# Kernel optimization log

Measured on AMD Instinct MI355X. Metric: run time of the kernel, lower is better.

Reference implementation:

```python
import jax, jax.numpy as jnp
import numpy as np

B, C, T = 8, 512, 1024
H = 8
D = C // H          # head_dim = 64
K = 64              # max_rel_dist
REL = 2 * K + 1     # 129


def setup_inputs() -> dict:
    key = jax.random.key(0)
    ks = jax.random.split(key, 12)
    s = 0.02
    return {
        "x": jax.random.normal(ks[0], (B, C, T), jnp.float32),
        "x_mask": jnp.ones((B, 1, T), jnp.float32),
        "W_q": jax.random.normal(ks[1], (C, C), jnp.float32) * s,
        "b_q": jnp.zeros((C,), jnp.float32),
        "W_k": jax.random.normal(ks[2], (C, C), jnp.float32) * s,
        "b_k": jnp.zeros((C,), jnp.float32),
        "W_v": jax.random.normal(ks[3], (C, C), jnp.float32) * s,
        "b_v": jnp.zeros((C,), jnp.float32),
        "W_o": jax.random.normal(ks[4], (C, C), jnp.float32) * s,
        "b_o": jnp.zeros((C,), jnp.float32),
        "emb_rel_k": jax.random.normal(ks[5], (REL, D), jnp.float32) * 0.01,
        "emb_rel_v": jax.random.normal(ks[6], (REL, D), jnp.float32) * 0.01,
    }


def _conv1x1(x, W, b):
    # Conv1d with kernel_size=1: (B,C,T) x (Cout,Cin) -> (B,Cout,T)
    return jnp.einsum("oc,bct->bot", W, x) + b[None, :, None]


def _shape_heads(x):
    # (B,C,T) -> (B,H,T,D)
    b = x.shape[0]
    return x.reshape(b, H, D, T).transpose(0, 1, 3, 2)


def reference(x, x_mask, W_q, b_q, W_k, b_k, W_v, b_v, W_o, b_o, emb_rel_k, emb_rel_v):
    q = _shape_heads(_conv1x1(x, W_q, b_q))  # (B,H,T,D)
    k = _shape_heads(_conv1x1(x, W_k, b_k))
    v = _shape_heads(_conv1x1(x, W_v, b_v))

    # relative position indices: clamp(j - i, -K, K) + K  -> (T,T)
    pos = jnp.arange(T)
    rel_idx = jnp.clip(pos[None, :] - pos[:, None], -K, K) + K

    # scores: scaled QK^T plus unscaled relative-key term (faithful to source)
    attn = jnp.einsum("bhid,bhjd->bhij", q, k) / (D ** 0.5)
    rel_k_tt = emb_rel_k[rel_idx]            # (T,T,D)
    attn = attn + jnp.einsum("bhid,ijd->bhij", q, rel_k_tt)

    # key mask: positions with x_mask <= 0 get -1e9
    key_mask = (x_mask <= 0).reshape(x.shape[0], 1, 1, T)
    attn = jnp.where(key_mask, -1e9, attn)
    attn = jax.nn.softmax(attn, axis=-1)     # dropout p=0.0 -> identity

    y = jnp.einsum("bhij,bhjd->bhid", attn, v)
    rel_v_tt = emb_rel_v[rel_idx]            # (T,T,D)
    y = y + jnp.einsum("bhij,ijd->bhid", attn, rel_v_tt)

    # (B,H,T,D) -> (B,H,D,T) -> (B,C,T)
    y = y.transpose(0, 1, 3, 2).reshape(x.shape[0], C, T)
    y = _conv1x1(y, W_o, b_o)
    return y * x_mask
```

## Files before the change

kernel.cpp:

```cpp
#include <hip/hip_runtime.h>

#define B_   8
#define C_   512
#define T_   1024
#define H_   8
#define D_   64
#define K_   64
#define REL_ 129

typedef unsigned short u16;
typedef __attribute__((ext_vector_type(8))) short short8;
typedef __attribute__((ext_vector_type(4))) float f32x4;

__device__ __forceinline__ float b2f(u16 u) {
    return __uint_as_float(((unsigned)u) << 16);
}
__device__ __forceinline__ u16 f2b(float f) {
    unsigned x = __float_as_uint(f);
    x += 0x7fffu + ((x >> 16) & 1u);
    return (u16)(x >> 16);
}

__global__ __launch_bounds__(256) void cast_all_kernel(
    const float* __restrict__ x,
    const float* __restrict__ Wq, const float* __restrict__ Wk,
    const float* __restrict__ Wv, const float* __restrict__ Wo,
    const float* __restrict__ erk, const float* __restrict__ erv,
    u16* __restrict__ xt, u16* __restrict__ Wh,
    u16* __restrict__ ervt, u16* __restrict__ erkb)
{
    __shared__ u16 tile[64][72];
    const int blk = blockIdx.x;
    const int tid = threadIdx.x;
    if (blk < 1024) {
        const int t0 = (blk & 15) * 64, c0 = ((blk >> 4) & 7) * 64, b = blk >> 7;
        const int f = tid & 15, r0 = tid >> 4;
#pragma unroll
        for (int p = 0; p < 4; ++p) {
            const int c = r0 + p * 16;
            const float4 v = *(const float4*)(x + ((size_t)b * C_ + c0 + c) * T_ + t0 + f * 4);
            tile[c][f * 4 + 0] = f2b(v.x);
            tile[c][f * 4 + 1] = f2b(v.y);
            tile[c][f * 4 + 2] = f2b(v.z);
            tile[c][f * 4 + 3] = f2b(v.w);
        }
        __syncthreads();
#pragma unroll
        for (int p = 0; p < 4; ++p) {
            const int t = r0 + p * 16;
            ushort4 u;
            u.x = tile[f * 4 + 0][t];
            u.y = tile[f * 4 + 1][t];
            u.z = tile[f * 4 + 2][t];
            u.w = tile[f * 4 + 3][t];
            *(ushort4*)(xt + ((size_t)b * T_ + t0 + t) * C_ + c0 + f * 4) = u;
        }
    } else if (blk < 2048) {
        const int gid = (blk - 1024) * 256 + tid;
        const int s = gid >> 16;
        const int off = (gid & 65535) * 4;
        const float* W = (s == 0) ? Wq : (s == 1) ? Wk : (s == 2) ? Wv : Wo;
        const float4 v = *(const float4*)(W + off);
        ushort4 u;
        u.x = f2b(v.x); u.y = f2b(v.y); u.z = f2b(v.z); u.w = f2b(v.w);
        *(ushort4*)(Wh + ((size_t)s << 18) + off) = u;
    } else {
        const int idx = (blk - 2048) * 256 + tid;
        if (idx < 64 * 160) {
            const int d = idx / 160, rel = idx % 160;
            ervt[idx] = (rel < REL_) ? f2b(erv[rel * D_ + d]) : (u16)0;
        } else {
            const int j = idx - 64 * 160;
            if (j < REL_ * D_) erkb[j] = f2b(erk[j]);
        }
    }
}

__global__ __launch_bounds__(256) void proj_mfma(
    const u16* __restrict__ xt, const u16* __restrict__ Wh,
    const float* __restrict__ bq, const float* __restrict__ bk, const float* __restrict__ bv,
    u16* __restrict__ qh, u16* __restrict__ kh, u16* __restrict__ vt)
{
    __shared__ u16 Wt[64][72];

    const int t0 = blockIdx.x * 128;
    const int h  = blockIdx.y;
    const int sel = blockIdx.z >> 3;
    const int b   = blockIdx.z & 7;
    const int tid = threadIdx.x, wave = tid >> 6, lane = tid & 63;
    const int quad = lane >> 4, l16 = lane & 15;

    const u16* Wbase = Wh + ((size_t)sel << 18) + ((size_t)(h * 64) << 9);
    const u16* A0 = xt + (((size_t)b * T_ + t0 + wave * 16 + l16) << 9);
    const u16* A1 = A0 + ((size_t)64 << 9);

    const int so = tid >> 2;
    const int sc = (tid & 3) * 16;
    const u16* wsrc = Wbase + ((size_t)so << 9) + sc;

    f32x4 acc[2][4];
#pragma unroll
    for (int gg = 0; gg < 2; ++gg)
#pragma unroll
        for (int nt = 0; nt < 4; ++nt) acc[gg][nt] = (f32x4){0.f, 0.f, 0.f, 0.f};

    uint4 wv0 = *(const uint4*)(wsrc);
    uint4 wv1 = *(const uint4*)(wsrc + 8);
#pragma unroll 1
    for (int i = 0; i < 8; ++i) {
        const int c0 = i * 64;
        __syncthreads();
        *(uint4*)&Wt[so][sc] = wv0;
        *(uint4*)&Wt[so][sc + 8] = wv1;
        __syncthreads();
        if (i < 7) {
            wv0 = *(const uint4*)(wsrc + c0 + 64);
            wv1 = *(const uint4*)(wsrc + c0 + 72);
        }
#pragma unroll
        for (int kk = 0; kk < 64; kk += 32) {
            const short8 af0 = *(const short8*)(A0 + c0 + kk + quad * 8);
            const short8 af1 = *(const short8*)(A1 + c0 + kk + quad * 8);
#pragma unroll
            for (int nt = 0; nt < 4; ++nt) {
                const short8 bf = *(const short8*)(&Wt[nt * 16 + l16][kk + quad * 8]);
                acc[0][nt] = __builtin_amdgcn_mfma_f32_16x16x32_bf16(af0, bf, acc[0][nt], 0, 0, 0);
                acc[1][nt] = __builtin_amdgcn_mfma_f32_16x16x32_bf16(af1, bf, acc[1][nt], 0, 0, 0);
            }
        }
    }

    const int bh = b * 8 + h;
    if (sel == 2) {
#pragma unroll
        for (int gg = 0; gg < 2; ++gg) {
            __syncthreads();
#pragma unroll
            for (int nt = 0; nt < 4; ++nt) {
                const int d = nt * 16 + l16;
                const float bo = bv[h * 64 + d];
#pragma unroll
                for (int rix = 0; rix < 4; ++rix) {
                    const int tl = wave * 16 + quad * 4 + rix;
                    Wt[d][tl] = f2b(acc[gg][nt][rix] + bo);
                }
            }
            __syncthreads();
            const int row = tid >> 2;
            const int seg = (tid & 3) * 16;
            const uint4 v0 = *(const uint4*)&Wt[row][seg];
            const uint4 v1 = *(const uint4*)&Wt[row][seg + 8];
            u16* vdst = vt + (((size_t)bh * 64 + row) << 10) + t0 + gg * 64 + seg;
            *(uint4*)(vdst) = v0;
            *(uint4*)(vdst + 8) = v1;
        }
    } else {
        const float* bias = sel ? bk : bq;
        u16* dst = sel ? kh : qh;
#pragma unroll
        for (int nt = 0; nt < 4; ++nt) {
            const int d = nt * 16 + l16;
            const float bo = bias[h * 64 + d];
#pragma unroll
            for (int gg = 0; gg < 2; ++gg)
#pragma unroll
                for (int rix = 0; rix < 4; ++rix) {
                    const int t = t0 + gg * 64 + wave * 16 + quad * 4 + rix;
                    dst[(((size_t)bh * T_ + t) << 6) + d] = f2b(acc[gg][nt][rix] + bo);
                }
        }
    }
}

__global__ __launch_bounds__(256, 2) void attn_kernel(
    const u16* __restrict__ qh, const u16* __restrict__ kh, const u16* __restrict__ vt,
    const u16* __restrict__ erkb, const u16* __restrict__ ervt,
    const float* __restrict__ xmask, u16* __restrict__ yf)
{
    __shared__ u16   Sb[32][1032];
    __shared__ u16   sw[32][168];
    __shared__ float red[4][32][2];
    __shared__ float invrow[32];

    const int gid = blockIdx.x;
    const int x8 = gid & 7, r5 = gid >> 3;
    const int bh = x8 + 8 * (r5 >> 5);
    const int i0 = (r5 & 31) * 32;
    const int b = bh >> 3, h = bh & 7;
    const int tid = threadIdx.x, wave = tid >> 6, lane = tid & 63;
    const int quad = lane >> 4, l16 = lane & 15;

    const float LOG2E = 1.4426950408889634f;
    const float SC    = 0.125f * 1.4426950408889634f;

    short8 qa[2][2];
#pragma unroll
    for (int g = 0; g < 2; ++g) {
        const u16* qrow = qh + (((size_t)bh * T_ + i0 + g * 16 + l16) << 6);
        qa[g][0] = *(const short8*)(qrow + quad * 8);
        qa[g][1] = *(const short8*)(qrow + 32 + quad * 8);
    }

    for (int tile = wave; tile < 9; tile += 4) {
        const int rel = tile * 16 + l16;
        const int rl = rel > 128 ? 128 : rel;
        const u16* ep = erkb + rl * 64 + quad * 8;
        const short8 b0 = *(const short8*)(ep);
        const short8 b1 = *(const short8*)(ep + 32);
#pragma unroll
        for (int g = 0; g < 2; ++g) {
            f32x4 m = {0.f, 0.f, 0.f, 0.f};
            m = __builtin_amdgcn_mfma_f32_16x16x32_bf16(qa[g][0], b0, m, 0, 0, 0);
            m = __builtin_amdgcn_mfma_f32_16x16x32_bf16(qa[g][1], b1, m, 0, 0, 0);
            if (rel < 129) {
#pragma unroll
                for (int rix = 0; rix < 4; ++rix)
                    sw[g * 16 + quad * 4 + rix][rel] = f2b(m[rix] * LOG2E);
            }
        }
    }
    __syncthreads();

    float slo_c[2][4], shi_c[2][4];
#pragma unroll
    for (int g = 0; g < 2; ++g)
#pragma unroll
        for (int rix = 0; rix < 4; ++rix) {
            const int row = g * 16 + quad * 4 + rix;
            slo_c[g][rix] = b2f(sw[row][0]);
            shi_c[g][rix] = b2f(sw[row][2 * K_]);
        }

    float psum[2][4] = {{0.f,0.f,0.f,0.f},{0.f,0.f,0.f,0.f}};
    float phi [2][4] = {{0.f,0.f,0.f,0.f},{0.f,0.f,0.f,0.f}};
    f32x4 og[4][2];
#pragma unroll
    for (int s = 0; s < 4; ++s)
#pragma unroll
        for (int g = 0; g < 2; ++g) og[s][g] = (f32x4){0.f, 0.f, 0.f, 0.f};

    {
        const u16* kb = kh + ((size_t)bh << 16);
        const u16* vbase = vt + ((size_t)bh << 16);

        short8 kc0, kc1;
        float  xmc;
        {
            const u16* krow0 = kb + ((size_t)(wave * 256 + l16) << 6);
            kc0 = *(const short8*)(krow0 + quad * 8);
            kc1 = *(const short8*)(krow0 + 32 + quad * 8);
            xmc = xmask[b * T_ + wave * 256 + l16];
        }
        short8 vaf[4];
#pragma unroll
        for (int s = 0; s < 4; ++s)
            vaf[s] = *(const short8*)(vbase + ((size_t)(s * 16 + l16) << 10) + wave * 256 + quad * 8);

#pragma unroll 1
        for (int c = 0; c < 8; ++c) {
#pragma unroll
            for (int half = 0; half < 2; ++half) {
                const int ct = c * 2 + half;
                const int j0 = wave * 256 + ct * 16;
                const int j = j0 + l16;
                const short8 kb0 = kc0, kb1 = kc1;
                const float xmv = xmc;
                {
                    const int jn = wave * 256 + ((ct < 15) ? ct + 1 : ct) * 16 + l16;
                    const u16* krown = kb + ((size_t)jn << 6);
                    kc0 = *(const short8*)(krown + quad * 8);
                    kc1 = *(const short8*)(krown + 32 + quad * 8);
                    xmc = xmask[b * T_ + jn];
                }
                const float clampv = (xmv > 0.f) ? 43.280850f : -2.0e9f;
#pragma unroll
                for (int g = 0; g < 2; ++g) {
                    f32x4 acc = {0.f, 0.f, 0.f, 0.f};
                    acc = __builtin_amdgcn_mfma_f32_16x16x32_bf16(qa[g][0], kb0, acc, 0, 0, 0);
                    acc = __builtin_amdgcn_mfma_f32_16x16x32_bf16(qa[g][1], kb1, acc, 0, 0, 0);
                    const int dd = j0 - (i0 + g * 16);
                    const int ibase = i0 + g * 16 + quad * 4;
                    float ee[4];
                    if (dd <= -79) {
#pragma unroll
                        for (int rix = 0; rix < 4; ++rix)
                            ee[rix] = __builtin_amdgcn_exp2f(
                                fminf(fmaf(acc[rix], SC, slo_c[g][rix]), clampv));
                    } else if (dd >= 79) {
#pragma unroll
                        for (int rix = 0; rix < 4; ++rix)
                            ee[rix] = __builtin_amdgcn_exp2f(
                                fminf(fmaf(acc[rix], SC, shi_c[g][rix]), clampv));
                    } else {
                        const int relb = j - ibase + K_;
#pragma unroll
                        for (int rix = 0; rix < 4; ++rix) {
                            int idx = relb - rix;
                            idx = idx < 0 ? 0 : (idx > 2 * K_ ? 2 * K_ : idx);
                            const int row = g * 16 + quad * 4 + rix;
                            const float sr = b2f(sw[row][idx]);
                            ee[rix] = __builtin_amdgcn_exp2f(
                                fminf(fmaf(acc[rix], SC, sr), clampv));
                        }
                    }
                    unsigned p01, p23;
                    asm("v_cvt_pk_bf16_f32 %0, %1, %2" : "=v"(p01) : "v"(ee[0]), "v"(ee[1]));
                    asm("v_cvt_pk_bf16_f32 %0, %1, %2" : "=v"(p23) : "v"(ee[2]), "v"(ee[3]));
                    const int r0 = g * 16 + quad * 4;
                    Sb[r0 + 0][j] = (u16)(p01 & 0xffffu);
                    Sb[r0 + 1][j] = (u16)(p01 >> 16);
                    Sb[r0 + 2][j] = (u16)(p23 & 0xffffu);
                    Sb[r0 + 3][j] = (u16)(p23 >> 16);
                    const float er0 = __uint_as_float(p01 << 16);
                    const float er1 = __uint_as_float(p01 & 0xffff0000u);
                    const float er2 = __uint_as_float(p23 << 16);
                    const float er3 = __uint_as_float(p23 & 0xffff0000u);
                    psum[g][0] += er0; psum[g][1] += er1;
                    psum[g][2] += er2; psum[g][3] += er3;
                    if (dd >= 79) {
                        phi[g][0] += er0; phi[g][1] += er1;
                        phi[g][2] += er2; phi[g][3] += er3;
                    } else if (dd > -79) {
                        phi[g][0] += (j - ibase >= 64) ? er0 : 0.f;
                        phi[g][1] += (j - ibase >= 65) ? er1 : 0.f;
                        phi[g][2] += (j - ibase >= 66) ? er2 : 0.f;
                        phi[g][3] += (j - ibase >= 67) ? er3 : 0.f;
                    }
                }
            }
            const int kc = wave * 256 + c * 32;
            const short8 pb0 = *(const short8*)(&Sb[l16][kc + quad * 8]);
            const short8 pb1 = *(const short8*)(&Sb[16 + l16][kc + quad * 8]);
            short8 vn[4];
            {
                const int kcn = wave * 256 + ((c < 7) ? c + 1 : c) * 32;
#pragma unroll
                for (int s = 0; s < 4; ++s)
                    vn[s] = *(const short8*)(vbase + ((size_t)(s * 16 + l16) << 10) + kcn + quad * 8);
            }
#pragma unroll
            for (int s = 0; s < 4; ++s) {
                og[s][0] = __builtin_amdgcn_mfma_f32_16x16x32_bf16(vaf[s], pb0, og[s][0], 0, 0, 0);
                og[s][1] = __builtin_amdgcn_mfma_f32_16x16x32_bf16(vaf[s], pb1, og[s][1], 0, 0, 0);
            }
#pragma unroll
            for (int s = 0; s < 4; ++s) vaf[s] = vn[s];
        }
#pragma unroll
        for (int m = 1; m < 16; m <<= 1)
#pragma unroll
            for (int g = 0; g < 2; ++g)
#pragma unroll
                for (int rix = 0; rix < 4; ++rix) {
                    psum[g][rix] += __shfl_xor(psum[g][rix], m);
                    phi[g][rix]  += __shfl_xor(phi[g][rix], m);
                }
        if (l16 == 0)
#pragma unroll
            for (int g = 0; g < 2; ++g)
#pragma unroll
                for (int rix = 0; rix < 4; ++rix) {
                    const int row = g * 16 + quad * 4 + rix;
                    red[wave][row][0] = psum[g][rix];
                    red[wave][row][1] = phi[g][rix];
                }
    }
    __syncthreads();

    {
        const int rr = tid >> 3;
        const int c0 = tid & 7;
        const float sumrow = red[0][rr][0] + red[1][rr][0] + red[2][rr][0] + red[3][rr][0];
        const float phirow = red[0][rr][1] + red[1][rr][1] + red[2][rr][1] + red[3][rr][1];
        float intsum = 0.f;
        for (int rel = c0; rel < 168; rel += 8) {
            if (rel == 0 || rel == 2 * K_) continue;
            u16 v = 0;
            if (rel < 2 * K_) {
                const int j = i0 + rr + rel - K_;
                if (j >= 0 && j < T_) v = Sb[rr][j];
                intsum += b2f(v);
            }
            sw[rr][rel] = v;
        }
        intsum += __shfl_xor(intsum, 1);
        intsum += __shfl_xor(intsum, 2);
        intsum += __shfl_xor(intsum, 4);
        if (c0 == 0) {
            sw[rr][2 * K_] = f2b(phirow);
            sw[rr][0]      = f2b(sumrow - intsum - phirow);
            invrow[rr]     = 1.0f / sumrow;
        }
    }
    __syncthreads();

    float* fog = (float*)&Sb[0][0];
#pragma unroll
    for (int s = 0; s < 4; ++s)
#pragma unroll
        for (int g = 0; g < 2; ++g)
            *(f32x4*)&fog[wave * 2048 + ((s * 2 + g) * 64 + lane) * 4] = og[s][g];
    __syncthreads();

    {
        const int dh = wave * 16 + l16;
        const u16* ep = ervt + dh * 160;
        f32x4 accg[2];
#pragma unroll
        for (int g = 0; g < 2; ++g) {
            const int base = ((wave * 2 + g) * 64 + lane) * 4;
            f32x4 a0 = *(const f32x4*)&fog[base];
            f32x4 a1 = *(const f32x4*)&fog[2048 + base];
            f32x4 a2 = *(const f32x4*)&fog[4096 + base];
            f32x4 a3 = *(const f32x4*)&fog[6144 + base];
#pragma unroll
            for (int rix = 0; rix < 4; ++rix)
                accg[g][rix] = (a0[rix] + a1[rix]) + (a2[rix] + a3[rix]);
        }
#pragma unroll
        for (int kt = 0; kt < 5; ++kt) {
            const short8 af = *(const short8*)(ep + kt * 32 + quad * 8);
            const short8 p0 = *(const short8*)(&sw[l16][kt * 32 + quad * 8]);
            const short8 p1 = *(const short8*)(&sw[16 + l16][kt * 32 + quad * 8]);
            accg[0] = __builtin_amdgcn_mfma_f32_16x16x32_bf16(af, p0, accg[0], 0, 0, 0);
            accg[1] = __builtin_amdgcn_mfma_f32_16x16x32_bf16(af, p1, accg[1], 0, 0, 0);
        }
        const int dbase = (h << 6) + wave * 16 + quad * 4;
#pragma unroll
        for (int g = 0; g < 2; ++g) {
            const float iv = invrow[g * 16 + l16];
            ushort4 u;
            u.x = f2b(accg[g][0] * iv); u.y = f2b(accg[g][1] * iv);
            u.z = f2b(accg[g][2] * iv); u.w = f2b(accg[g][3] * iv);
            *(ushort4*)(yf + (((size_t)b * T_ + i0 + g * 16 + l16) << 9) + dbase) = u;
        }
    }
}

__global__ __launch_bounds__(256) void outproj_mfma(
    const u16* __restrict__ yf, const u16* __restrict__ Woh, const float* __restrict__ bo,
    const float* __restrict__ xmask, float* __restrict__ out)
{
    __shared__ u16 Yt[64][72];

    const int o0 = blockIdx.x * 64;
    const int b  = blockIdx.y >> 4;
    const int t0 = (blockIdx.y & 15) * 64;
    const int tid = threadIdx.x, wave = tid >> 6, lane = tid & 63;
    const int quad = lane >> 4, l16 = lane & 15;

    const u16* A = Woh + ((size_t)(o0 + wave * 16 + l16) << 9);

    const int so = tid >> 2;
    const int sc = (tid & 3) * 16;
    const u16* ysrc = yf + (((size_t)b * T_ + t0 + so) << 9) + sc;

    f32x4 acc[4] = {{0.f,0.f,0.f,0.f},{0.f,0.f,0.f,0.f},{0.f,0.f,0.f,0.f},{0.f,0.f,0.f,0.f}};

    uint4 wv0 = *(const uint4*)(ysrc);
    uint4 wv1 = *(const uint4*)(ysrc + 8);
#pragma unroll 1
    for (int i = 0; i < 8; ++i) {
        const int c0 = i * 64;
        __syncthreads();
        *(uint4*)&Yt[so][sc] = wv0;
        *(uint4*)&Yt[so][sc + 8] = wv1;
        __syncthreads();
        if (i < 7) {
            wv0 = *(const uint4*)(ysrc + c0 + 64);
            wv1 = *(const uint4*)(ysrc + c0 + 72);
        }
#pragma unroll
        for (int kk = 0; kk < 64; kk += 32) {
            const short8 af = *(const short8*)(A + c0 + kk + quad * 8);
#pragma unroll
            for (int nt = 0; nt < 4; ++nt) {
                const short8 bf = *(const short8*)(&Yt[nt * 16 + l16][kk + quad * 8]);
                acc[nt] = __builtin_amdgcn_mfma_f32_16x16x32_bf16(af, bf, acc[nt], 0, 0, 0);
            }
        }
    }

#pragma unroll
    for (int nt = 0; nt < 4; ++nt) {
        const int t = t0 + nt * 16 + l16;
        const float xmv = xmask[b * T_ + t];
#pragma unroll
        for (int rix = 0; rix < 4; ++rix) {
            const int o = o0 + wave * 16 + quad * 4 + rix;
            out[((size_t)b * C_ + o) * T_ + t] = (acc[nt][rix] + bo[o]) * xmv;
        }
    }
}

extern "C" void kernel_launch(void* const* d_in, const int* in_sizes, int n_in,
                              void* d_out, int out_size, void* d_ws, size_t ws_size,
                              hipStream_t stream) {
    const float* x     = (const float*)d_in[0];
    const float* xmask = (const float*)d_in[1];
    const float* Wq    = (const float*)d_in[2];
    const float* bq    = (const float*)d_in[3];
    const float* Wk    = (const float*)d_in[4];
    const float* bk    = (const float*)d_in[5];
    const float* Wv    = (const float*)d_in[6];
    const float* bv    = (const float*)d_in[7];
    const float* Wo    = (const float*)d_in[8];
    const float* bo    = (const float*)d_in[9];
    const float* erk   = (const float*)d_in[10];
    const float* erv   = (const float*)d_in[11];

    const size_t need = 44077184;
    if (ws_size < need) return;
    u16* xt   = (u16*)d_ws;
    u16* Wh   = (u16*)((char*)d_ws + 8388608);
    u16* qh   = (u16*)((char*)d_ws + 10485760);
    u16* kh   = (u16*)((char*)d_ws + 18874368);
    u16* vt   = (u16*)((char*)d_ws + 27262976);
    u16* yf   = (u16*)((char*)d_ws + 35651584);
    u16* ervt = (u16*)((char*)d_ws + 44040192);
    u16* erkb = (u16*)((char*)d_ws + 44060672);
    float* out = (float*)d_out;

    cast_all_kernel<<<dim3(2121), 256, 0, stream>>>(
        x, Wq, Wk, Wv, Wo, erk, erv, xt, Wh, ervt, erkb);
    proj_mfma<<<dim3(T_ / 128, H_, 3 * B_), 256, 0, stream>>>(
        xt, Wh, bq, bk, bv, qh, kh, vt);
    attn_kernel<<<dim3(2048), 256, 0, stream>>>(
        qh, kh, vt, erkb, ervt, xmask, yf);
    outproj_mfma<<<dim3(C_ / 64, B_ * (T_ / 64)), 256, 0, stream>>>(
        yf, Wh + ((size_t)3 << 18), bo, xmask, out);
}
```

Baseline: 225.4 us.

## Replace full-row score buffer with per-wave chunk and band buffers for occupancy

Drops the large per-block LDS buffer that held every bf16 probability for 32 rows × 1024 keys. It replaces it with a small per-wave chunk buffer feeding the PV MFMA, plus a 129-wide band buffer that keeps only the relative-position window needed for the rel-v term. The smaller LDS footprint allows the launch bound to rise from 2 to 3 blocks per CU, aiming at better latency hiding. The cross-wave output reduction is now serialized into one shared buffer, which adds four barriers. The tighter register budget may cause spills.

```diff
diff --git a/kernel.cpp b/kernel.cpp
--- a/kernel.cpp
+++ b/kernel.cpp
@@ -172,13 +172,15 @@
     }
 }
 
-__global__ __launch_bounds__(256, 2) void attn_kernel(
+__global__ __launch_bounds__(256, 3) void attn_kernel(
     const u16* __restrict__ qh, const u16* __restrict__ kh, const u16* __restrict__ vt,
     const u16* __restrict__ erkb, const u16* __restrict__ ervt,
     const float* __restrict__ xmask, u16* __restrict__ yf)
 {
-    __shared__ u16   Sb[32][1032];
     __shared__ u16   sw[32][168];
+    __shared__ u16   bandbuf[32][136];
+    __shared__ u16   chunkbuf[4][32][40];
+    __shared__ float ogbuf[32][68];
     __shared__ float red[4][32][2];
     __shared__ float invrow[32];
 
@@ -192,6 +194,12 @@
 
     const float LOG2E = 1.4426950408889634f;
     const float SC    = 0.125f * 1.4426950408889634f;
+
+    {
+        unsigned* bb = (unsigned*)&bandbuf[0][0];
+#pragma unroll 1
+        for (int k2 = tid; k2 < 32 * 68; k2 += 256) bb[k2] = 0u;
+    }
 
     short8 qa[2][2];
 #pragma unroll
@@ -280,6 +288,8 @@
                     acc = __builtin_amdgcn_mfma_f32_16x16x32_bf16(qa[g][1], kb1, acc, 0, 0, 0);
                     const int dd = j0 - (i0 + g * 16);
                     const int ibase = i0 + g * 16 + quad * 4;
+                    const int relb = j - ibase + K_;
+                    const bool interior = (dd > -79) && (dd < 79);
                     float ee[4];
                     if (dd <= -79) {
 #pragma unroll
@@ -292,7 +302,6 @@
                             ee[rix] = __builtin_amdgcn_exp2f(
                                 fminf(fmaf(acc[rix], SC, shi_c[g][rix]), clampv));
                     } else {
-                        const int relb = j - ibase + K_;
 #pragma unroll
                         for (int rix = 0; rix < 4; ++rix) {
                             int idx = relb - rix;
@@ -307,10 +316,21 @@
                     asm("v_cvt_pk_bf16_f32 %0, %1, %2" : "=v"(p01) : "v"(ee[0]), "v"(ee[1]));
                     asm("v_cvt_pk_bf16_f32 %0, %1, %2" : "=v"(p23) : "v"(ee[2]), "v"(ee[3]));
                     const int r0 = g * 16 + quad * 4;
-                    Sb[r0 + 0][j] = (u16)(p01 & 0xffffu);
-                    Sb[r0 + 1][j] = (u16)(p01 >> 16);
-                    Sb[r0 + 2][j] = (u16)(p23 & 0xffffu);
-                    Sb[r0 + 3][j] = (u16)(p23 >> 16);
+                    const int ccol = half * 16 + l16;
+                    const u16 pv0 = (u16)(p01 & 0xffffu);
+                    const u16 pv1 = (u16)(p01 >> 16);
+                    const u16 pv2 = (u16)(p23 & 0xffffu);
+                    const u16 pv3 = (u16)(p23 >> 16);
+                    chunkbuf[wave][r0 + 0][ccol] = pv0;
+                    chunkbuf[wave][r0 + 1][ccol] = pv1;
+                    chunkbuf[wave][r0 + 2][ccol] = pv2;
+                    chunkbuf[wave][r0 + 3][ccol] = pv3;
+                    if (interior) {
+                        if ((unsigned)(relb - 1) < 127u) bandbuf[r0 + 0][relb]     = pv0;
+                        if ((unsigned)(relb - 2) < 127u) bandbuf[r0 + 1][relb - 1] = pv1;
+                        if ((unsigned)(relb - 3) < 127u) bandbuf[r0 + 2][relb - 2] = pv2;
+                        if ((unsigned)(relb - 4) < 127u) bandbuf[r0 + 3][relb - 3] = pv3;
+                    }
                     const float er0 = __uint_as_float(p01 << 16);
                     const float er1 = __uint_as_float(p01 & 0xffff0000u);
                     const float er2 = __uint_as_float(p23 << 16);
@@ -328,9 +348,8 @@
                     }
                 }
             }
-            const int kc = wave * 256 + c * 32;
-            const short8 pb0 = *(const short8*)(&Sb[l16][kc + quad * 8]);
-            const short8 pb1 = *(const short8*)(&Sb[16 + l16][kc + quad * 8]);
+            const short8 pb0 = *(const short8*)(&chunkbuf[wave][l16][quad * 8]);
+            const short8 pb1 = *(const short8*)(&chunkbuf[wave][16 + l16][quad * 8]);
             short8 vn[4];
             {
                 const int kcn = wave * 256 + ((c < 7) ? c + 1 : c) * 32;
@@ -377,8 +396,7 @@
             if (rel == 0 || rel == 2 * K_) continue;
             u16 v = 0;
             if (rel < 2 * K_) {
-                const int j = i0 + rr + rel - K_;
-                if (j >= 0 && j < T_) v = Sb[rr][j];
+                v = bandbuf[rr][rel];
                 intsum += b2f(v);
             }
             sw[rr][rel] = v;
@@ -394,29 +412,36 @@
     }
     __syncthreads();
 
-    float* fog = (float*)&Sb[0][0];
-#pragma unroll
-    for (int s = 0; s < 4; ++s)
-#pragma unroll
-        for (int g = 0; g < 2; ++g)
-            *(f32x4*)&fog[wave * 2048 + ((s * 2 + g) * 64 + lane) * 4] = og[s][g];
-    __syncthreads();
+#pragma unroll
+    for (int w = 0; w < 4; ++w) {
+        if (wave == w) {
+            if (w == 0) {
+#pragma unroll
+                for (int s = 0; s < 4; ++s)
+#pragma unroll
+                    for (int g = 0; g < 2; ++g)
+                        *(f32x4*)&ogbuf[g * 16 + l16][s * 16 + quad * 4] = og[s][g];
+            } else {
+#pragma unroll
+                for (int s = 0; s < 4; ++s)
+#pragma unroll
+                    for (int g = 0; g < 2; ++g) {
+                        f32x4 cur = *(const f32x4*)&ogbuf[g * 16 + l16][s * 16 + quad * 4];
+                        cur = cur + og[s][g];
+                        *(f32x4*)&ogbuf[g * 16 + l16][s * 16 + quad * 4] = cur;
+                    }
+            }
+        }
+        __syncthreads();
+    }
 
     {
         const int dh = wave * 16 + l16;
         const u16* ep = ervt + dh * 160;
         f32x4 accg[2];
 #pragma unroll
-        for (int g = 0; g < 2; ++g) {
-            const int base = ((wave * 2 + g) * 64 + lane) * 4;
-            f32x4 a0 = *(const f32x4*)&fog[base];
-            f32x4 a1 = *(const f32x4*)&fog[2048 + base];
-            f32x4 a2 = *(const f32x4*)&fog[4096 + base];
-            f32x4 a3 = *(const f32x4*)&fog[6144 + base];
-#pragma unroll
-            for (int rix = 0; rix < 4; ++rix)
-                accg[g][rix] = (a0[rix] + a1[rix]) + (a2[rix] + a3[rix]);
-        }
+        for (int g = 0; g < 2; ++g)
+            accg[g] = *(const f32x4*)&ogbuf[g * 16 + l16][wave * 16 + quad * 4];
 #pragma unroll
         for (int kt = 0; kt < 5; ++kt) {
             const short8 af = *(const short8*)(ep + kt * 32 + quad * 8);
```

New measurement: 214.4 us. 1.05x faster.
